# Kernel optimization log

Measured on AMD Instinct MI355X. Metric: run time of the kernel, lower is better.

Reference implementation:

```python
import jax, jax.numpy as jnp
import numpy as np
from jax import lax

NH = 8          # heads
DK = 64         # total key/query depth
DV = 64         # total value depth
DKH = DK // NH  # per-head key depth = 8
DVH = DV // NH  # per-head value depth = 8
H = W = 32
CIN = 256
FILTERS = 256


def rel_to_abs(x):
    # x: [B, N, L, 2L-1] relative logits -> [B, N, L, L] absolute logits
    B, N, L, _ = x.shape
    x = jnp.pad(x, ((0, 0), (0, 0), (0, 0), (0, 1)))          # [B,N,L,2L]
    flat = x.reshape(B, N, L * 2 * L)
    flat = jnp.pad(flat, ((0, 0), (0, 0), (0, L - 1)))        # [B,N,2L^2+L-1]
    final = flat.reshape(B, N, L + 1, 2 * L - 1)
    return final[:, :, :L, L - 1:]


def rel_logits_1d(q, rel_k, h, w, perm):
    # q: [B, NH, h, w, DKH], rel_k: [2w-1, DKH]
    B = q.shape[0]
    rel = jnp.einsum('bnxyd,md->bnxym', q, rel_k)             # [B,NH,h,w,2w-1]
    rel = rel.reshape(B, NH * h, w, 2 * w - 1)
    rel = rel_to_abs(rel)                                     # [B,NH*h,w,w]
    rel = rel.reshape(B, NH, h, w, w)[:, :, :, None]          # [B,NH,h,1,w,w]
    rel = jnp.broadcast_to(rel, (B, NH, h, h, w, w))          # tile over other axis
    rel = jnp.transpose(rel, perm)
    return rel.reshape(B, NH, h * w, h * w)


def setup_inputs() -> dict:
    key = jax.random.key(0)
    ks = jax.random.split(key, 6)
    s = lambda fan_in: 1.0 / np.sqrt(fan_in)
    return {
        'x': jax.random.normal(ks[0], (8, H, W, CIN), jnp.float32),
        'conv_w': jax.random.normal(ks[1], (3, 3, CIN, FILTERS - DV), jnp.float32) * s(9 * CIN),
        'conv_b': jnp.zeros((FILTERS - DV,), jnp.float32),
        'qkv_w': jax.random.normal(ks[2], (CIN, 2 * DK + DV), jnp.float32) * s(CIN),
        'qkv_b': jnp.zeros((2 * DK + DV,), jnp.float32),
        'attn_w': jax.random.normal(ks[3], (DV, DV), jnp.float32) * s(DV),
        'attn_b': jnp.zeros((DV,), jnp.float32),
        'key_rel_w': jax.random.normal(ks[4], (2 * W - 1, DKH), jnp.float32),
        'key_rel_h': jax.random.normal(ks[5], (2 * H - 1, DKH), jnp.float32),
    }


def reference(x, conv_w, conv_b, qkv_w, qkv_b, attn_w, attn_b, key_rel_w, key_rel_h):
    B = x.shape[0]
    # standard conv branch (SAME padding)
    conv_out = lax.conv_general_dilated(
        x, conv_w, window_strides=(1, 1), padding='SAME',
        dimension_numbers=('NHWC', 'HWIO', 'NHWC')) + conv_b

    # 1x1 qkv projection
    kqv = jnp.einsum('bhwc,co->bhwo', x, qkv_w) + qkv_b
    k = kqv[..., :DK]
    q = kqv[..., DK:2 * DK] * (DKH ** -0.5)
    v = kqv[..., 2 * DK:]

    def split_heads(t, d):
        return t.reshape(B, H, W, NH, d).transpose(0, 3, 1, 2, 4)  # [B,NH,H,W,d]

    qh = split_heads(q, DKH)
    kh = split_heads(k, DKH)
    vh = split_heads(v, DVH)

    qf = qh.reshape(B, NH, H * W, DKH)
    kf = kh.reshape(B, NH, H * W, DKH)
    vf = vh.reshape(B, NH, H * W, DVH)

    logits = jnp.einsum('bnid,bnjd->bnij', qf, kf)            # [B,NH,HW,HW]
    rel_w = rel_logits_1d(qh, key_rel_w, H, W, (0, 1, 2, 4, 3, 5))
    qh_t = qh.transpose(0, 1, 3, 2, 4)                        # [B,NH,W,H,d]
    rel_h = rel_logits_1d(qh_t, key_rel_h, W, H, (0, 1, 4, 2, 5, 3))
    logits = logits + rel_w + rel_h

    weights = jax.nn.softmax(logits, axis=-1)
    attn = jnp.einsum('bnij,bnjd->bnid', weights, vf)         # [B,NH,HW,DVH]
    attn = attn.reshape(B, NH, H, W, DVH).transpose(0, 2, 3, 1, 4).reshape(B, H, W, DV)
    attn = jnp.einsum('bhwc,co->bhwo', attn, attn_w) + attn_b

    return jnp.concatenate([conv_out, attn], axis=3)
```

## Files before the change

### kernel.cpp

```cpp
#include <hip/hip_runtime.h>
#include <cstdint>

using u16 = unsigned short;
using u32 = uint32_t;

typedef __attribute__((ext_vector_type(8))) short bf16x8;
typedef __attribute__((ext_vector_type(4))) float f32x4;

__device__ __forceinline__ float bf2f(u16 v) { return __uint_as_float(((u32)v) << 16); }
__device__ __forceinline__ u16 f2bf(float f) {
    u32 u = __float_as_uint(f);
    u += 0x7fffu + ((u >> 16) & 1u);
    return (u16)(u >> 16);
}
__device__ __forceinline__ u16 bf16u(float f) {
#if defined(__BF16_MANT_DIG__)
    __bf16 h = (__bf16)f;
    return __builtin_bit_cast(u16, h);
#else
    return f2bf(f);
#endif
}
__device__ __forceinline__ float fexp2(float x) {
#if __has_builtin(__builtin_amdgcn_exp2f)
    return __builtin_amdgcn_exp2f(x);
#else
    float r; asm("v_exp_f32 %0, %1" : "=v"(r) : "v"(x)); return r;
#endif
}

#define FLAG_OFF 0
#define ZERO_OFF 8
#define WSH_OFF  2097168
#define AWF_OFF  2588688
#define CBF_OFF  2592784
#define QBF_OFF  2592976
#define ABF_OFF  2593168
#define KRW_OFF  2593232
#define KRH_OFF  2593736
#define KB_OFF   2594240
#define QB_OFF   3118528
#define VB_OFF   3642816
#define AT_OFF   4167104
#define XBF_OFF  4691392
#define WSHQ_OFF 9409984

__global__ void detect_kernel(const u16* __restrict__ x, int* __restrict__ flag) {
    __shared__ int cnt;
    if (threadIdx.x == 0) cnt = 0;
    __syncthreads();
    int c = 0;
    #pragma unroll
    for (int k = 0; k < 16; k++) {
        u16 v = x[threadIdx.x * 16 + k];
        int e = (v >> 7) & 0xFF;
        c += (e >= 110 && e <= 140) ? 1 : 0;
    }
    atomicAdd(&cnt, c);
    __syncthreads();
    if (threadIdx.x == 0) *flag = (cnt > 3300) ? 1 : 0;
}

__global__ __launch_bounds__(256) void xcvt_kernel(
    const void* __restrict__ xr, u16* __restrict__ xbf, const int* __restrict__ flag)
{
    const int g = blockIdx.x * 256 + threadIdx.x;
    if (*flag) {
        *(uint4*)(xbf + (size_t)g * 8) = *(const uint4*)((const u16*)xr + (size_t)g * 8);
    } else {
        const float* src = (const float*)xr + (size_t)g * 8;
        float4 a = *(const float4*)src, b = *(const float4*)(src + 4);
        uint4 o;
        o.x = (u32)f2bf(a.x) | ((u32)f2bf(a.y) << 16);
        o.y = (u32)f2bf(a.z) | ((u32)f2bf(a.w) << 16);
        o.z = (u32)f2bf(b.x) | ((u32)f2bf(b.y) << 16);
        o.w = (u32)f2bf(b.z) | ((u32)f2bf(b.w) << 16);
        *(uint4*)(xbf + (size_t)g * 8) = o;
    }
}

__global__ __launch_bounds__(256) void prep_kernel(
    const void* __restrict__ cw, const void* __restrict__ qw,
    const void* __restrict__ cb, const void* __restrict__ qb,
    const void* __restrict__ aw, const void* __restrict__ ab,
    const void* __restrict__ kw_, const void* __restrict__ kh_,
    u16* __restrict__ wshC, u16* __restrict__ wshQ,
    float* __restrict__ cbf, float* __restrict__ qbf, float* __restrict__ awf,
    float* __restrict__ abf, float* __restrict__ krw, float* __restrict__ krh,
    float* __restrict__ zbuf, const int* __restrict__ flag)
{
    const int blk = blockIdx.x;
    const int fl = *flag;
    if (blk < 240) {
        const void* w; u16* o; int g;
        if (blk < 216) { w = cw; o = wshC; g = blk * 256 + threadIdx.x; }
        else           { w = qw; o = wshQ; g = (blk - 216) * 256 + threadIdx.x; }
        const int kk = g / 768, rem = g % 768;
        const int tile = rem >> 6, lane = rem & 63;
        const int n = tile * 16 + (lane & 15);
        u16 tmp[8];
        #pragma unroll
        for (int j = 0; j < 8; j++) {
            const size_t k = (size_t)(kk * 32 + ((lane >> 4) << 3) + j);
            tmp[j] = fl ? ((const u16*)w)[k * 192 + n]
                        : f2bf(((const float*)w)[k * 192 + n]);
        }
        *(uint4*)(o + (size_t)g * 8) = *(const uint4*)tmp;
    } else {
        const int gid = (blk - 240) * 256 + threadIdx.x;
        const void* src; float* dst; int e;
        if      (gid <  192) { src = cb;  dst = cbf; e = gid; }
        else if (gid <  384) { src = qb;  dst = qbf; e = gid - 192; }
        else if (gid < 4480) { src = aw;  dst = awf; e = gid - 384; }
        else if (gid < 4544) { src = ab;  dst = abf; e = gid - 4480; }
        else if (gid < 5048) { src = kw_; dst = krw; e = gid - 4544; }
        else if (gid < 5552) { src = kh_; dst = krh; e = gid - 5048; }
        else if (gid < 5568) { zbuf[gid - 5552] = 0.f; return; }
        else return;
        dst[e] = fl ? bf2f(((const u16*)src)[e]) : ((const float*)src)[e];
    }
}

__global__ __launch_bounds__(256) void qkv_mfma_kernel(
    const u16* __restrict__ xbf, const u16* __restrict__ wsh, const float* __restrict__ qbf_,
    u16* __restrict__ kb16, float* __restrict__ qbuf, u16* __restrict__ vb16)
{
    const int coh = blockIdx.x, row = blockIdx.y;
    const int b = row >> 5, h = row & 31;
    const int t = threadIdx.x;
    __shared__ u16 xs[32 * 264];

    {
        const u16* src = xbf + (size_t)row * 8192;
        #pragma unroll
        for (int i = 0; i < 4; ++i) {
            const int idx = t + i * 256;
            const int px = idx >> 5, cq = idx & 31;
            *(uint4*)(xs + px * 264 + cq * 8) = *(const uint4*)(src + px * 256 + cq * 8);
        }
    }
    __syncthreads();

    const int lane = t & 63, wave = t >> 6;
    const int Mtile = wave & 1;
    const int tg0 = coh * 6 + (wave >> 1) * 3;
    const int l15 = lane & 15, quad = lane >> 4;

    f32x4 acc[3] = {{0,0,0,0},{0,0,0,0},{0,0,0,0}};

    const u16* ap = xs + (Mtile * 16 + l15) * 264 + quad * 8;
    #pragma unroll
    for (int kk = 0; kk < 8; ++kk) {
        const bf16x8 av = *(const bf16x8*)(ap + kk * 32);
        const u16* wp = wsh + ((size_t)(kk * 12 + tg0) * 64 + lane) * 8;
        const bf16x8 b0 = *(const bf16x8*)(wp);
        const bf16x8 b1 = *(const bf16x8*)(wp + 512);
        const bf16x8 b2 = *(const bf16x8*)(wp + 1024);
        acc[0] = __builtin_amdgcn_mfma_f32_16x16x32_bf16(av, b0, acc[0], 0, 0, 0);
        acc[1] = __builtin_amdgcn_mfma_f32_16x16x32_bf16(av, b1, acc[1], 0, 0, 0);
        acc[2] = __builtin_amdgcn_mfma_f32_16x16x32_bf16(av, b2, acc[2], 0, 0, 0);
    }

    const int px0 = Mtile * 16 + quad * 4;
    #pragma unroll
    for (int ti = 0; ti < 3; ++ti) {
        const int tg = tg0 + ti;
        const int o = tg * 16 + l15;
        const int third = tg >> 2;
        const int within = o - third * 64;
        const int n = within >> 3, d = within & 7;
        const float bias = qbf_[o];
        #pragma unroll
        for (int r = 0; r < 4; ++r) {
            const int i = h * 32 + px0 + r;
            const size_t off = ((size_t)(b * 8 + n) * 1024 + i) * 8 + d;
            const float val = acc[ti][r] + bias;
            if (third == 0)      kb16[off] = f2bf(val);
            else if (third == 1) qbuf[off] = val * 0.51006973050f;
            else                 vb16[off] = f2bf(val);
        }
    }
}

__global__ __launch_bounds__(256) void conv_mfma_kernel(
    const u16* __restrict__ xbf, const u16* __restrict__ wsh, const float* __restrict__ cbf,
    const int* __restrict__ flag, void* __restrict__ out)
{
    const int coh = blockIdx.x, row = blockIdx.y;
    const int b = row >> 5, h = row & 31;
    const int t = threadIdx.x;
    __shared__ u16 xs[3 * 34 * 264];
    const int fl = *flag;

    #pragma unroll
    for (int r = 0; r < 3; ++r) {
        const int hh = h + r - 1;
        if (t < 64) {
            const int s = (t >> 5) ? 33 : 0, cq = t & 31;
            *(uint4*)(xs + (r * 34 + s) * 264 + cq * 8) = make_uint4(0, 0, 0, 0);
        }
        const bool ok = (hh >= 0) && (hh < 32);
        const u16* src = xbf + ((size_t)((b * 32 + (ok ? hh : 0)) * 32)) * 256;
        #pragma unroll
        for (int i = 0; i < 4; ++i) {
            const int idx = t + i * 256;
            const int px = idx >> 5, cq = idx & 31;
            uint4 v = ok ? *(const uint4*)(src + px * 256 + cq * 8)
                         : make_uint4(0, 0, 0, 0);
            *(uint4*)(xs + (r * 34 + 1 + px) * 264 + cq * 8) = v;
        }
    }
    __syncthreads();

    const int lane = t & 63, wave = t >> 6;
    const int Mtile = wave & 1;
    const int tg0 = coh * 6 + (wave >> 1) * 3;
    const int l15 = lane & 15, quad = lane >> 4;

    f32x4 acc[3] = {{0,0,0,0},{0,0,0,0},{0,0,0,0}};

    #pragma unroll
    for (int p = 0; p < 9; ++p) {
        const int kh = p / 3, kw = p - kh * 3;
        const u16* ap = xs + (kh * 34 + kw + Mtile * 16 + l15) * 264 + quad * 8;
        #pragma unroll
        for (int ck = 0; ck < 8; ++ck) {
            const int kk = p * 8 + ck;
            const bf16x8 av = *(const bf16x8*)(ap + ck * 32);
            const u16* wp = wsh + ((size_t)(kk * 12 + tg0) * 64 + lane) * 8;
            const bf16x8 b0 = *(const bf16x8*)(wp);
            const bf16x8 b1 = *(const bf16x8*)(wp + 512);
            const bf16x8 b2 = *(const bf16x8*)(wp + 1024);
            acc[0] = __builtin_amdgcn_mfma_f32_16x16x32_bf16(av, b0, acc[0], 0, 0, 0);
            acc[1] = __builtin_amdgcn_mfma_f32_16x16x32_bf16(av, b1, acc[1], 0, 0, 0);
            acc[2] = __builtin_amdgcn_mfma_f32_16x16x32_bf16(av, b2, acc[2], 0, 0, 0);
        }
    }

    const int px0 = Mtile * 16 + quad * 4;
    #pragma unroll
    for (int ti = 0; ti < 3; ++ti) {
        const int co = (tg0 + ti) * 16 + l15;
        const float bias = cbf[co];
        #pragma unroll
        for (int r = 0; r < 4; ++r) {
            const size_t oidx = ((size_t)row * 32 + px0 + r) * 256 + co;
            const float v = acc[ti][r] + bias;
            if (fl) ((u16*)out)[oidx] = f2bf(v);
            else    ((float*)out)[oidx] = v;
        }
    }
}

#define ATTN_STEP8(C, KA, KB, OACC)                                            \
  do {                                                                         \
    const int c_ = (C);                                                        \
    const float rhv = sRH[c_ * 68 + wave * 16 + l15];                          \
    f32x4 acc0, acc1;                                                          \
    acc0[0] = rhv + rw0[0]; acc0[1] = rhv + rw0[1];                            \
    acc0[2] = rhv + rw0[2]; acc0[3] = rhv + rw0[3];                            \
    acc1[0] = rhv + rw1[0]; acc1[1] = rhv + rw1[1];                            \
    acc1[2] = rhv + rw1[2]; acc1[3] = rhv + rw1[3];                            \
    acc0 = __builtin_amdgcn_mfma_f32_16x16x32_bf16(KA, Aq.v, acc0, 0, 0, 0);   \
    acc1 = __builtin_amdgcn_mfma_f32_16x16x32_bf16(KB, Aq.v, acc1, 0, 0, 0);   \
    if (c_ + 2 < 32) {                \
      KA = *(const bf16x8*)(kp0 + (c_ + 2) * 256);                             \
      KB = *(const bf16x8*)(kp1 + (c_ + 2) * 256);                             \
    }                                                                          \
    union { u16 a[8]; bf16x8 v; } pf;                                          \
    pf.a[0] = bf16u(fexp2(fminf(acc0[0], 80.0f)));                             \
    pf.a[1] = bf16u(fexp2(fminf(acc0[1], 80.0f)));                             \
    pf.a[2] = bf16u(fexp2(fminf(acc0[2], 80.0f)));                             \
    pf.a[3] = bf16u(fexp2(fminf(acc0[3], 80.0f)));                             \
    pf.a[4] = bf16u(fexp2(fminf(acc1[0], 80.0f)));                             \
    pf.a[5] = bf16u(fexp2(fminf(acc1[1], 80.0f)));                             \
    pf.a[6] = bf16u(fexp2(fminf(acc1[2], 80.0f)));                             \
    pf.a[7] = bf16u(fexp2(fminf(acc1[3], 80.0f)));                             \
    bf16x8 Av;                                                                 \
    if (l15 < 8) Av = *(const bf16x8*)(sVT + l15 * 1032 + c_ * 32 + quad * 8); \
    else         Av = ONE.v;                                                   \
    OACC = __builtin_amdgcn_mfma_f32_16x16x32_bf16(Av, pf.v, OACC, 0, 0, 0);   \
  } while (0)

__global__ __launch_bounds__(256) void attn_mfma_kernel(
    const u16* __restrict__ kb16, const float* __restrict__ qbuf, const u16* __restrict__ vb16,
    const float* __restrict__ krw, const float* __restrict__ krh,
    float* __restrict__ attnbuf)
{
    const int qb = blockIdx.x;
    const int bn = blockIdx.y;
    const int b = bn >> 3, hn = bn & 7;
    const int t = threadIdx.x;
    const int i0 = qb * 64;

    __shared__ __align__(16) u16   sVT[8 * 1032];
    __shared__ __align__(16) u16   sRW[64 * 40];
    __shared__ __align__(16) float sRH[32 * 68];

    const u16* vg = vb16 + (size_t)bn * 8192;
    #pragma unroll
    for (int k4 = 0; k4 < 4; k4++) {
        const int key = t + k4 * 256;
        uint4 vv = *(const uint4*)(vg + key * 8);
        sVT[0 * 1032 + key] = (u16)(vv.x);  sVT[1 * 1032 + key] = (u16)(vv.x >> 16);
        sVT[2 * 1032 + key] = (u16)(vv.y);  sVT[3 * 1032 + key] = (u16)(vv.y >> 16);
        sVT[4 * 1032 + key] = (u16)(vv.z);  sVT[5 * 1032 + key] = (u16)(vv.z >> 16);
        sVT[6 * 1032 + key] = (u16)(vv.w);  sVT[7 * 1032 + key] = (u16)(vv.w >> 16);
    }
    #pragma unroll
    for (int k8 = 0; k8 < 8; k8++) {
        const int idx = t + k8 * 256;
        const int il = idx >> 5, w = idx & 31;
        const int i = i0 + il;
        const float* q = qbuf + ((size_t)bn * 1024 + i) * 8;
        float4 qa = *(const float4*)q, qc = *(const float4*)(q + 4);
        const float* rp = krw + (size_t)(w - (i & 31) + 31) * 8;
        float4 ra = *(const float4*)rp, rc = *(const float4*)(rp + 4);
        sRW[il * 40 + w] = f2bf(qa.x*ra.x + qa.y*ra.y + qa.z*ra.z + qa.w*ra.w
                              + qc.x*rc.x + qc.y*rc.y + qc.z*rc.z + qc.w*rc.w);
        const float* hp = krh + (size_t)(w - (i >> 5) + 31) * 8;
        float4 ha = *(const float4*)hp, hc = *(const float4*)(hp + 4);
        sRH[w * 68 + il] = qa.x*ha.x + qa.y*ha.y + qa.z*ha.z + qa.w*ha.w
                         + qc.x*hc.x + qc.y*hc.y + qc.z*hc.z + qc.w*hc.w;
    }
    __syncthreads();

    const int lane = t & 63, wave = t >> 6;
    const int l15 = lane & 15, quad = lane >> 4;

    union Frag { u16 a[8]; bf16x8 v; };
    Frag Aq;
    {
        const float* q = qbuf + ((size_t)bn * 1024 + i0 + wave * 16 + l15) * 8;
        float4 qa = *(const float4*)q, qc = *(const float4*)(q + 4);
        Aq.a[0] = f2bf(qa.x); Aq.a[1] = f2bf(qa.y); Aq.a[2] = f2bf(qa.z); Aq.a[3] = f2bf(qa.w);
        Aq.a[4] = f2bf(qc.x); Aq.a[5] = f2bf(qc.y); Aq.a[6] = f2bf(qc.z); Aq.a[7] = f2bf(qc.w);
        if (quad != 0) {
            #pragma unroll
            for (int j = 0; j < 8; j++) Aq.a[j] = 0;
        }
    }
    const bf16x8 Arw = *(const bf16x8*)(sRW + (wave * 16 + l15) * 40 + quad * 8);

    Frag S0, S1, ONE;
    #pragma unroll
    for (int j = 0; j < 8; j++) { S0.a[j] = 0; S1.a[j] = 0; ONE.a[j] = 0x3F80; }
    if (quad == (l15 >> 2)) {
        S0.a[l15 & 3]       = 0x3F80;
        S1.a[4 + (l15 & 3)] = 0x3F80;
    }

    f32x4 zero4 = {0.f, 0.f, 0.f, 0.f};
    const f32x4 rw0 = __builtin_amdgcn_mfma_f32_16x16x32_bf16(S0.v, Arw, zero4, 0, 0, 0);
    const f32x4 rw1 = __builtin_amdgcn_mfma_f32_16x16x32_bf16(S1.v, Arw, zero4, 0, 0, 0);

    const u16* kg = kb16 + (size_t)bn * 8192;
    const int s = l15 >> 2, rr = l15 & 3;
    const u16* kp0 = kg + (size_t)(8 * s + rr) * 8;
    const u16* kp1 = kg + (size_t)(8 * s + 4 + rr) * 8;

    f32x4 oaccE = {0.f, 0.f, 0.f, 0.f};
    f32x4 oaccO = {0.f, 0.f, 0.f, 0.f};

    bf16x8 kAa = *(const bf16x8*)(kp0);
    bf16x8 kBa = *(const bf16x8*)(kp1);
    bf16x8 kAb = *(const bf16x8*)(kp0 + 256);
    bf16x8 kBb = *(const bf16x8*)(kp1 + 256);

    for (int c2 = 0; c2 < 32; c2 += 2) {
        ATTN_STEP8(c2,     kAa, kBa, oaccE);
        ATTN_STEP8(c2 + 1, kAb, kBb, oaccO);
    }

    f32x4 oacc;
    oacc[0] = oaccE[0] + oaccO[0];
    oacc[1] = oaccE[1] + oaccO[1];
    oacc[2] = oaccE[2] + oaccO[2];
    oacc[3] = oaccE[3] + oaccO[3];

    const float lr = __shfl(oacc[0], 32 + l15, 64);
    const float inv = 1.0f / fmaxf(lr, 1e-30f);
    if (quad < 2) {
        float4 o;
        o.x = oacc[0] * inv; o.y = oacc[1] * inv;
        o.z = oacc[2] * inv; o.w = oacc[3] * inv;
        *(float4*)(attnbuf + ((size_t)b * 1024 + i0 + wave * 16 + l15) * 64
                   + hn * 8 + quad * 4) = o;
    }
}

__global__ __launch_bounds__(256) void proj_kernel(
    const float* __restrict__ attnbuf, const float* __restrict__ awf, const float* __restrict__ abf,
    const int* __restrict__ flag, void* __restrict__ out)
{
    const int g = blockIdx.x * 256 + threadIdx.x;
    const int px = g >> 6, o = g & 63;
    const float* ar = attnbuf + (size_t)px * 64;
    float acc = abf[o];
    #pragma unroll 8
    for (int c = 0; c < 64; c++) acc += ar[c] * awf[c * 64 + o];
    if (*flag) ((u16*)out)[(size_t)px * 256 + 192 + o] = f2bf(acc);
    else       ((float*)out)[(size_t)px * 256 + 192 + o] = acc;
}

extern "C" void kernel_launch(void* const* d_in, const int* in_sizes, int n_in,
                              void* d_out, int out_size, void* d_ws, size_t ws_size,
                              hipStream_t stream)
{
    float* ws = (float*)d_ws;
    int*   flag = (int*)(ws + FLAG_OFF);
    float* zbuf = ws + ZERO_OFF;
    u16*   wsh  = (u16*)(ws + WSH_OFF);
    float* awf  = ws + AWF_OFF;
    float* cbf  = ws + CBF_OFF;
    float* qbf  = ws + QBF_OFF;
    float* abf  = ws + ABF_OFF;
    float* krw  = ws + KRW_OFF;
    float* krh  = ws + KRH_OFF;
    u16*   kb16 = (u16*)(ws + KB_OFF);
    float* qbuf = ws + QB_OFF;
    u16*   vb16 = (u16*)(ws + VB_OFF);
    float* atb  = ws + AT_OFF;
    u16*   xbf  = (u16*)(ws + XBF_OFF);
    u16*   wshQ = (u16*)(ws + WSHQ_OFF);

    detect_kernel<<<1, 256, 0, stream>>>((const u16*)d_in[0], flag);

    prep_kernel<<<262, 256, 0, stream>>>(
        d_in[1], d_in[3], d_in[2], d_in[4], d_in[5], d_in[6], d_in[7], d_in[8],
        wsh, wshQ, cbf, qbf, awf, abf, krw, krh, zbuf, flag);

    xcvt_kernel<<<1024, 256, 0, stream>>>(d_in[0], xbf, flag);

    qkv_mfma_kernel <<<dim3(2, 256), 256, 0, stream>>>(xbf, wshQ, qbf, kb16, qbuf, vb16);
    conv_mfma_kernel<<<dim3(2, 256), 256, 0, stream>>>(xbf, wsh, cbf, flag, d_out);
    attn_mfma_kernel<<<dim3(16, 64), 256, 0, stream>>>(kb16, qbuf, vb16, krw, krh, atb);
    proj_kernel     <<<2048,         256, 0, stream>>>(atb, awf, abf, flag, d_out);
}
```

Before: 165.3 us.

## Split attention key loop across wave pairs and reduce partial sums in LDS

Each attention block now handles 32 queries instead of 64, and the grid doubles to 2048 blocks. Two waves share each 16-query group and each processes half of the key chunks (interleaved by sub-wave index). Their partial output and denominator accumulators are combined through shared memory before normalisation. The aim is more parallelism and occupancy for the softmax-V loop, at the cost of reloading the V transpose into LDS twice as often per head and adding an extra barrier and reduction.

New measurement: 164.0 us. About the same (-0.8%).

```diff
diff --git a/kernel.cpp b/kernel.cpp
--- a/kernel.cpp
+++ b/kernel.cpp
@@ -252,10 +252,10 @@
     }
 }
 
-#define ATTN_STEP8(C, KA, KB, OACC)                                            \
+#define ATTN_STEPA(C, KA, KB, OACC)                                            \
   do {                                                                         \
     const int c_ = (C);                                                        \
-    const float rhv = sRH[c_ * 68 + wave * 16 + l15];                          \
+    const float rhv = sRH[c_ * 36 + pair * 16 + l15];                          \
     f32x4 acc0, acc1;                                                          \
     acc0[0] = rhv + rw0[0]; acc0[1] = rhv + rw0[1];                            \
     acc0[2] = rhv + rw0[2]; acc0[3] = rhv + rw0[3];                            \
@@ -263,9 +263,9 @@
     acc1[2] = rhv + rw1[2]; acc1[3] = rhv + rw1[3];                            \
     acc0 = __builtin_amdgcn_mfma_f32_16x16x32_bf16(KA, Aq.v, acc0, 0, 0, 0);   \
     acc1 = __builtin_amdgcn_mfma_f32_16x16x32_bf16(KB, Aq.v, acc1, 0, 0, 0);   \
-    if (c_ + 2 < 32) {                \
-      KA = *(const bf16x8*)(kp0 + (c_ + 2) * 256);                             \
-      KB = *(const bf16x8*)(kp1 + (c_ + 2) * 256);                             \
+    if (c_ + 4 < 32) {                \
+      KA = *(const bf16x8*)(kp0 + (c_ + 4) * 256);                             \
+      KB = *(const bf16x8*)(kp1 + (c_ + 4) * 256);                             \
     }                                                                          \
     union { u16 a[8]; bf16x8 v; } pf;                                          \
     pf.a[0] = bf16u(fexp2(fminf(acc0[0], 80.0f)));                             \
@@ -291,11 +291,12 @@
     const int bn = blockIdx.y;
     const int b = bn >> 3, hn = bn & 7;
     const int t = threadIdx.x;
-    const int i0 = qb * 64;
+    const int i0 = qb * 32;
 
     __shared__ __align__(16) u16   sVT[8 * 1032];
-    __shared__ __align__(16) u16   sRW[64 * 40];
-    __shared__ __align__(16) float sRH[32 * 68];
+    __shared__ __align__(16) u16   sRW[32 * 40];
+    __shared__ __align__(16) float sRH[32 * 36];
+    __shared__ __align__(16) float sRed[2 * 64 * 4];
 
     const u16* vg = vb16 + (size_t)bn * 8192;
     #pragma unroll
@@ -308,7 +309,7 @@
         sVT[6 * 1032 + key] = (u16)(vv.w);  sVT[7 * 1032 + key] = (u16)(vv.w >> 16);
     }
     #pragma unroll
-    for (int k8 = 0; k8 < 8; k8++) {
+    for (int k8 = 0; k8 < 4; k8++) {
         const int idx = t + k8 * 256;
         const int il = idx >> 5, w = idx & 31;
         const int i = i0 + il;
@@ -320,18 +321,19 @@
                               + qc.x*rc.x + qc.y*rc.y + qc.z*rc.z + qc.w*rc.w);
         const float* hp = krh + (size_t)(w - (i >> 5) + 31) * 8;
         float4 ha = *(const float4*)hp, hc = *(const float4*)(hp + 4);
-        sRH[w * 68 + il] = qa.x*ha.x + qa.y*ha.y + qa.z*ha.z + qa.w*ha.w
+        sRH[w * 36 + il] = qa.x*ha.x + qa.y*ha.y + qa.z*ha.z + qa.w*ha.w
                          + qc.x*hc.x + qc.y*hc.y + qc.z*hc.z + qc.w*hc.w;
     }
     __syncthreads();
 
     const int lane = t & 63, wave = t >> 6;
+    const int pair = wave >> 1, sub = wave & 1;
     const int l15 = lane & 15, quad = lane >> 4;
 
     union Frag { u16 a[8]; bf16x8 v; };
     Frag Aq;
     {
-        const float* q = qbuf + ((size_t)bn * 1024 + i0 + wave * 16 + l15) * 8;
+        const float* q = qbuf + ((size_t)bn * 1024 + i0 + pair * 16 + l15) * 8;
         float4 qa = *(const float4*)q, qc = *(const float4*)(q + 4);
         Aq.a[0] = f2bf(qa.x); Aq.a[1] = f2bf(qa.y); Aq.a[2] = f2bf(qa.z); Aq.a[3] = f2bf(qa.w);
         Aq.a[4] = f2bf(qc.x); Aq.a[5] = f2bf(qc.y); Aq.a[6] = f2bf(qc.z); Aq.a[7] = f2bf(qc.w);
@@ -340,7 +342,7 @@
             for (int j = 0; j < 8; j++) Aq.a[j] = 0;
         }
     }
-    const bf16x8 Arw = *(const bf16x8*)(sRW + (wave * 16 + l15) * 40 + quad * 8);
+    const bf16x8 Arw = *(const bf16x8*)(sRW + (pair * 16 + l15) * 40 + quad * 8);
 
     Frag S0, S1, ONE;
     #pragma unroll
@@ -362,14 +364,14 @@
     f32x4 oaccE = {0.f, 0.f, 0.f, 0.f};
     f32x4 oaccO = {0.f, 0.f, 0.f, 0.f};
 
-    bf16x8 kAa = *(const bf16x8*)(kp0);
-    bf16x8 kBa = *(const bf16x8*)(kp1);
-    bf16x8 kAb = *(const bf16x8*)(kp0 + 256);
-    bf16x8 kBb = *(const bf16x8*)(kp1 + 256);
-
-    for (int c2 = 0; c2 < 32; c2 += 2) {
-        ATTN_STEP8(c2,     kAa, kBa, oaccE);
-        ATTN_STEP8(c2 + 1, kAb, kBb, oaccO);
+    bf16x8 kAa = *(const bf16x8*)(kp0 + sub * 256);
+    bf16x8 kBa = *(const bf16x8*)(kp1 + sub * 256);
+    bf16x8 kAb = *(const bf16x8*)(kp0 + (sub + 2) * 256);
+    bf16x8 kBb = *(const bf16x8*)(kp1 + (sub + 2) * 256);
+
+    for (int c2 = sub; c2 < 32; c2 += 4) {
+        ATTN_STEPA(c2,     kAa, kBa, oaccE);
+        ATTN_STEPA(c2 + 2, kAb, kBb, oaccO);
     }
 
     f32x4 oacc;
@@ -378,14 +380,22 @@
     oacc[2] = oaccE[2] + oaccO[2];
     oacc[3] = oaccE[3] + oaccO[3];
 
-    const float lr = __shfl(oacc[0], 32 + l15, 64);
-    const float inv = 1.0f / fmaxf(lr, 1e-30f);
-    if (quad < 2) {
-        float4 o;
-        o.x = oacc[0] * inv; o.y = oacc[1] * inv;
-        o.z = oacc[2] * inv; o.w = oacc[3] * inv;
-        *(float4*)(attnbuf + ((size_t)b * 1024 + i0 + wave * 16 + l15) * 64
-                   + hn * 8 + quad * 4) = o;
+    if (sub == 1) *(f32x4*)(sRed + (pair * 64 + lane) * 4) = oacc;
+    __syncthreads();
+    if (sub == 0) {
+        const f32x4 part = *(const f32x4*)(sRed + (pair * 64 + lane) * 4);
+        oacc[0] += part[0]; oacc[1] += part[1];
+        oacc[2] += part[2]; oacc[3] += part[3];
+
+        const float lr = __shfl(oacc[0], 32 + l15, 64);
+        const float inv = 1.0f / fmaxf(lr, 1e-30f);
+        if (quad < 2) {
+            float4 o;
+            o.x = oacc[0] * inv; o.y = oacc[1] * inv;
+            o.z = oacc[2] * inv; o.w = oacc[3] * inv;
+            *(float4*)(attnbuf + ((size_t)b * 1024 + i0 + pair * 16 + l15) * 64
+                       + hn * 8 + quad * 4) = o;
+        }
     }
 }
 
@@ -434,6 +444,6 @@
 
     qkv_mfma_kernel <<<dim3(2, 256), 256, 0, stream>>>(xbf, wshQ, qbf, kb16, qbuf, vb16);
     conv_mfma_kernel<<<dim3(2, 256), 256, 0, stream>>>(xbf, wsh, cbf, flag, d_out);
-    attn_mfma_kernel<<<dim3(16, 64), 256, 0, stream>>>(kb16, qbuf, vb16, krw, krh, atb);
+    attn_mfma_kernel<<<dim3(32, 64), 256, 0, stream>>>(kb16, qbuf, vb16, krw, krh, atb);
     proj_kernel     <<<2048,         256, 0, stream>>>(atb, awf, abf, flag, d_out);
 }
```
